# Kernel optimization log

Hardware: AMD Instinct MI355X
Metric: run time of the kernel (lower is better)

Reference implementation:

```python
import jax, jax.numpy as jnp
import numpy as np

N, K, M, DIM = 131072, 16, 128, 64


def setup_inputs() -> dict:
    key = jax.random.key(0)
    kx, ks, ka, kb = jax.random.split(key, 4)
    return {
        "x": jax.random.normal(kx, (N, DIM), dtype=jnp.float32),
        "s": jax.random.normal(ks, (K,), dtype=jnp.float32),
        "a": jax.random.normal(ka, (K, M, DIM), dtype=jnp.float32),
        "b": jax.random.normal(kb, (K, M), dtype=jnp.float32),
    }


def reference(x, s, a, b):
    # scores[k, n, m] = x[n, :] @ a[k, m, :] + b[k, m]  (batched GEMM over k)
    scores = jnp.einsum("nd,kmd->knm", x, a) + b[:, None, :]
    # per-expert logsumexp over the m affine pieces -> [k, n]
    lse = jax.nn.logsumexp(scores, axis=-1)
    # signed sum over experts -> [n]
    return jnp.einsum("k,kn->n", s, lse)
```

## Files before the change

kernel.cpp:

```cpp
#include <hip/hip_runtime.h>
#include <hip/hip_bf16.h>

#define NROWS 131072
#define KEXP 16
#define MPC 128
#define DIMD 64

typedef float f32x4  __attribute__((ext_vector_type(4)));
typedef float f32x16 __attribute__((ext_vector_type(16)));
typedef short s16x8  __attribute__((ext_vector_type(8)));

#define L2E 1.4426950408889634f
#define LN2 0.6931471805599453f

static __device__ inline unsigned int b2u(__hip_bfloat162 h) {
    union { __hip_bfloat162 h; unsigned int u; } c;
    c.h = h;
    return c.u;
}

static __device__ inline int4 cvt8s(float4 f0, float4 f1, float sc) {
    __hip_bfloat162 p0 = __float22bfloat162_rn(make_float2(f0.x * sc, f0.y * sc));
    __hip_bfloat162 p1 = __float22bfloat162_rn(make_float2(f0.z * sc, f0.w * sc));
    __hip_bfloat162 p2 = __float22bfloat162_rn(make_float2(f1.x * sc, f1.y * sc));
    __hip_bfloat162 p3 = __float22bfloat162_rn(make_float2(f1.z * sc, f1.w * sc));
    int4 pk;
    pk.x = (int)b2u(p0); pk.y = (int)b2u(p1); pk.z = (int)b2u(p2); pk.w = (int)b2u(p3);
    return pk;
}

__global__ __launch_bounds__(256, 2)
void fused_kernel(const float* __restrict__ x, const float* __restrict__ s,
                  const float* __restrict__ a, const float* __restrict__ b,
                  float* __restrict__ out) {
    __shared__ int4  abuf[2][1024];
    __shared__ float lb[KEXP * MPC];

    const int tid  = threadIdx.x;
    const int w    = tid >> 6;
    const int l    = tid & 63;
    const int ln   = l & 31;
    const int half = l >> 5;

    const int r0 = blockIdx.x * 256 + w * 64;

    {
        const float* bp = b + tid * 8;
        float4 b0 = *(const float4*)(bp);
        float4 b1 = *(const float4*)(bp + 4);
        float4 o0 = {b0.x * L2E, b0.y * L2E, b0.z * L2E, b0.w * L2E};
        float4 o1 = {b1.x * L2E, b1.y * L2E, b1.z * L2E, b1.w * L2E};
        *(float4*)(lb + tid * 8)     = o0;
        *(float4*)(lb + tid * 8 + 4) = o1;
    }

    union { int4 i; s16x8 v; } Bf[2][4];
#pragma unroll
    for (int nt = 0; nt < 2; ++nt)
#pragma unroll
        for (int c = 0; c < 4; ++c) {
            const float* gp = x + (size_t)(r0 + nt * 32 + ln) * DIMD + c * 16 + half * 8;
            float4 f0 = *(const float4*)(gp);
            float4 f1 = *(const float4*)(gp + 4);
            Bf[nt][c].i = cvt8s(f0, f1, 1.0f);
        }

#pragma unroll
    for (int i = 0; i < 4; ++i) {
        const int u  = i * 256 + tid;
        const int fb = u >> 6;
        const int ul = u & 63;
        const float* p = a + (size_t)((fb >> 2) * 32 + (ul & 31)) * DIMD
                           + (fb & 3) * 16 + (ul >> 5) * 8;
        float4 f0 = *(const float4*)(p);
        float4 f1 = *(const float4*)(p + 4);
        abuf[0][u] = cvt8s(f0, f1, L2E);
    }
    __syncthreads();

    float racc0 = 0.f, racc1 = 0.f;

    for (int k = 0; k < KEXP; ++k) {
        float4 ga[8];
        if (k + 1 < KEXP) {
            const float* ap = a + (size_t)(k + 1) * MPC * DIMD;
#pragma unroll
            for (int i = 0; i < 4; ++i) {
                const int u  = i * 256 + tid;
                const int fb = u >> 6;
                const int ul = u & 63;
                const float* p = ap + (size_t)((fb >> 2) * 32 + (ul & 31)) * DIMD
                                    + (fb & 3) * 16 + (ul >> 5) * 8;
                ga[i * 2]     = *(const float4*)(p);
                ga[i * 2 + 1] = *(const float4*)(p + 4);
            }
        }

        const int   kb  = k & 1;
        const float sk2 = s[k] * LN2;
        float esum0 = 0.f, esum1 = 0.f;

#pragma unroll
        for (int mt = 0; mt < 4; ++mt) {
            f32x4 lbv[4];
#pragma unroll
            for (int g = 0; g < 4; ++g)
                lbv[g] = *(const f32x4*)(lb + k * MPC + mt * 32 + g * 8 + half * 4);

            s16x8 Af[4];
#pragma unroll
            for (int c = 0; c < 4; ++c)
                Af[c] = *(const s16x8*)&abuf[kb][mt * 256 + c * 64 + l];

            f32x16 acc0, acc1;
#pragma unroll
            for (int g = 0; g < 4; ++g)
#pragma unroll
                for (int j = 0; j < 4; ++j) {
                    acc0[g * 4 + j] = lbv[g][j];
                    acc1[g * 4 + j] = lbv[g][j];
                }
#pragma unroll
            for (int c = 0; c < 4; ++c)
                acc0 = __builtin_amdgcn_mfma_f32_32x32x16_bf16(Af[c], Bf[0][c].v, acc0, 0, 0, 0);
#pragma unroll
            for (int c = 0; c < 4; ++c)
                acc1 = __builtin_amdgcn_mfma_f32_32x32x16_bf16(Af[c], Bf[1][c].v, acc1, 0, 0, 0);

            float e0 = 0.f, e1 = 0.f;
            {
                float t0[8], t1[8];
#pragma unroll
                for (int r = 0; r < 8; ++r) {
                    t0[r] = __builtin_amdgcn_exp2f(acc0[2 * r]) + __builtin_amdgcn_exp2f(acc0[2 * r + 1]);
                    t1[r] = __builtin_amdgcn_exp2f(acc1[2 * r]) + __builtin_amdgcn_exp2f(acc1[2 * r + 1]);
                }
#pragma unroll
                for (int r = 0; r < 4; ++r) { t0[r] += t0[r + 4]; t1[r] += t1[r + 4]; }
                e0 = (t0[0] + t0[1]) + (t0[2] + t0[3]);
                e1 = (t1[0] + t1[1]) + (t1[2] + t1[3]);
            }
            esum0 += e0;
            esum1 += e1;
        }

        float tot0 = esum0 + __shfl_xor(esum0, 32);
        float tot1 = esum1 + __shfl_xor(esum1, 32);
        racc0 = fmaf(sk2, __log2f(tot0), racc0);
        racc1 = fmaf(sk2, __log2f(tot1), racc1);

        if (k + 1 < KEXP) {
#pragma unroll
            for (int i = 0; i < 4; ++i)
                abuf[kb ^ 1][i * 256 + tid] = cvt8s(ga[i * 2], ga[i * 2 + 1], L2E);
        }
        __syncthreads();
    }

    out[r0 + l] = half ? racc1 : racc0;
}

extern "C" void kernel_launch(void* const* d_in, const int* in_sizes, int n_in,
                              void* d_out, int out_size, void* d_ws, size_t ws_size,
                              hipStream_t stream) {
    const float* x = (const float*)d_in[0];
    const float* s = (const float*)d_in[1];
    const float* a = (const float*)d_in[2];
    const float* b = (const float*)d_in[3];
    float* out = (float*)d_out;

    fused_kernel<<<NROWS / 256, 256, 0, stream>>>(x, s, a, b, out);
}
```

Measured before the change: 135.1 us.

## Pre-convert expert weights once and split experts across two block families

Adds a prep kernel that converts the expert matrices `a` to pre-swizzled bf16 (scaled by log2 e) and prescales `b` into a workspace, so the main kernel no longer converts fp32 weights per block. The main kernel streams this bf16 data into LDS with async global-to-LDS copies. It also splits the 16 experts across two block families per row tile, doubling the grid and raising the occupancy hint, and combines the two partial sums with atomicAdd after a memset of the output. This trades redundant conversion work for an extra launch, a memset, the atomics, and the x tile being read and converted twice.

```diff
diff --git a/kernel.cpp b/kernel.cpp
--- a/kernel.cpp
+++ b/kernel.cpp
@@ -29,9 +29,40 @@
     return pk;
 }
 
-__global__ __launch_bounds__(256, 2)
+static __device__ inline void async_copy16(const void* g, void* l) {
+    __builtin_amdgcn_global_load_lds(
+        (const __attribute__((address_space(1))) unsigned int*)g,
+        (__attribute__((address_space(3))) unsigned int*)l, 16, 0, 0);
+}
+
+__global__ void prep_kernel(const float* __restrict__ a, const float* __restrict__ b,
+                            short* __restrict__ abff, float* __restrict__ lbf) {
+    if (blockIdx.x < 64) {
+        const int u   = blockIdx.x * 256 + threadIdx.x;
+        const int k   = u >> 10;
+        const int rem = u & 1023;
+        const int fb  = rem >> 6;
+        const int ul  = rem & 63;
+        const int mt  = fb >> 2, c = fb & 3;
+        const float* p = a + (size_t)(k * MPC + mt * 32 + (ul & 31)) * DIMD
+                           + c * 16 + (ul >> 5) * 8;
+        float4 f0 = *(const float4*)(p);
+        float4 f1 = *(const float4*)(p + 4);
+        *(int4*)(abff + (size_t)u * 8) = cvt8s(f0, f1, L2E);
+    } else {
+        const int t = threadIdx.x;
+        float4 v0 = *(const float4*)(b + t * 8);
+        float4 v1 = *(const float4*)(b + t * 8 + 4);
+        float4 o0 = {v0.x * L2E, v0.y * L2E, v0.z * L2E, v0.w * L2E};
+        float4 o1 = {v1.x * L2E, v1.y * L2E, v1.z * L2E, v1.w * L2E};
+        *(float4*)(lbf + t * 8)     = o0;
+        *(float4*)(lbf + t * 8 + 4) = o1;
+    }
+}
+
+__global__ __launch_bounds__(256, 4)
 void fused_kernel(const float* __restrict__ x, const float* __restrict__ s,
-                  const float* __restrict__ a, const float* __restrict__ b,
+                  const short* __restrict__ abff, const float* __restrict__ lbf,
                   float* __restrict__ out) {
     __shared__ int4  abuf[2][1024];
     __shared__ float lb[KEXP * MPC];
@@ -42,16 +73,14 @@
     const int ln   = l & 31;
     const int half = l >> 5;
 
-    const int r0 = blockIdx.x * 256 + w * 64;
+    const int family = blockIdx.x & 1;
+    const int r0w    = (blockIdx.x >> 1) * 256 + w * 64;
 
     {
-        const float* bp = b + tid * 8;
-        float4 b0 = *(const float4*)(bp);
-        float4 b1 = *(const float4*)(bp + 4);
-        float4 o0 = {b0.x * L2E, b0.y * L2E, b0.z * L2E, b0.w * L2E};
-        float4 o1 = {b1.x * L2E, b1.y * L2E, b1.z * L2E, b1.w * L2E};
-        *(float4*)(lb + tid * 8)     = o0;
-        *(float4*)(lb + tid * 8 + 4) = o1;
+        float4 v0 = *(const float4*)(lbf + tid * 8);
+        float4 v1 = *(const float4*)(lbf + tid * 8 + 4);
+        *(float4*)(lb + tid * 8)     = v0;
+        *(float4*)(lb + tid * 8 + 4) = v1;
     }
 
     union { int4 i; s16x8 v; } Bf[2][4];
@@ -59,89 +88,74 @@
     for (int nt = 0; nt < 2; ++nt)
 #pragma unroll
         for (int c = 0; c < 4; ++c) {
-            const float* gp = x + (size_t)(r0 + nt * 32 + ln) * DIMD + c * 16 + half * 8;
+            const float* gp = x + (size_t)(r0w + nt * 32 + ln) * DIMD + c * 16 + half * 8;
             float4 f0 = *(const float4*)(gp);
             float4 f1 = *(const float4*)(gp + 4);
             Bf[nt][c].i = cvt8s(f0, f1, 1.0f);
         }
 
+    {
+        const short* src = abff + (size_t)(family * 8) * 8192;
 #pragma unroll
-    for (int i = 0; i < 4; ++i) {
-        const int u  = i * 256 + tid;
-        const int fb = u >> 6;
-        const int ul = u & 63;
-        const float* p = a + (size_t)((fb >> 2) * 32 + (ul & 31)) * DIMD
-                           + (fb & 3) * 16 + (ul >> 5) * 8;
-        float4 f0 = *(const float4*)(p);
-        float4 f1 = *(const float4*)(p + 4);
-        abuf[0][u] = cvt8s(f0, f1, L2E);
+        for (int i = 0; i < 4; ++i) {
+            const int chunk = w * 4 + i;
+            async_copy16(src + chunk * 512 + l * 8,
+                         (char*)&abuf[0][0] + chunk * 1024);
+        }
     }
     __syncthreads();
 
     float racc0 = 0.f, racc1 = 0.f;
 
-    for (int k = 0; k < KEXP; ++k) {
-        float4 ga[8];
-        if (k + 1 < KEXP) {
-            const float* ap = a + (size_t)(k + 1) * MPC * DIMD;
+    for (int k = 0; k < 8; ++k) {
+        const int kf = family * 8 + k;
+        const int kb = k & 1;
+
+        if (k + 1 < 8) {
+            const short* src = abff + (size_t)(kf + 1) * 8192;
 #pragma unroll
             for (int i = 0; i < 4; ++i) {
-                const int u  = i * 256 + tid;
-                const int fb = u >> 6;
-                const int ul = u & 63;
-                const float* p = ap + (size_t)((fb >> 2) * 32 + (ul & 31)) * DIMD
-                                    + (fb & 3) * 16 + (ul >> 5) * 8;
-                ga[i * 2]     = *(const float4*)(p);
-                ga[i * 2 + 1] = *(const float4*)(p + 4);
+                const int chunk = w * 4 + i;
+                async_copy16(src + chunk * 512 + l * 8,
+                             (char*)&abuf[kb ^ 1][0] + chunk * 1024);
             }
         }
 
-        const int   kb  = k & 1;
-        const float sk2 = s[k] * LN2;
+        const float sk2 = s[kf] * LN2;
         float esum0 = 0.f, esum1 = 0.f;
 
 #pragma unroll
         for (int mt = 0; mt < 4; ++mt) {
-            f32x4 lbv[4];
-#pragma unroll
-            for (int g = 0; g < 4; ++g)
-                lbv[g] = *(const f32x4*)(lb + k * MPC + mt * 32 + g * 8 + half * 4);
-
             s16x8 Af[4];
 #pragma unroll
             for (int c = 0; c < 4; ++c)
-                Af[c] = *(const s16x8*)&abuf[kb][mt * 256 + c * 64 + l];
+                Af[c] = *(const s16x8*)((const short*)&abuf[kb][0] + (mt * 4 + c) * 512 + l * 8);
 
-            f32x16 acc0, acc1;
+            union { f32x4 q[4]; f32x16 v; } acc_a, acc_b;
 #pragma unroll
-            for (int g = 0; g < 4; ++g)
-#pragma unroll
-                for (int j = 0; j < 4; ++j) {
-                    acc0[g * 4 + j] = lbv[g][j];
-                    acc1[g * 4 + j] = lbv[g][j];
-                }
+            for (int g = 0; g < 4; ++g) {
+                f32x4 t = *(const f32x4*)(lb + kf * MPC + mt * 32 + g * 8 + half * 4);
+                acc_a.q[g] = t;
+                acc_b.q[g] = t;
+            }
+
 #pragma unroll
             for (int c = 0; c < 4; ++c)
-                acc0 = __builtin_amdgcn_mfma_f32_32x32x16_bf16(Af[c], Bf[0][c].v, acc0, 0, 0, 0);
+                acc_a.v = __builtin_amdgcn_mfma_f32_32x32x16_bf16(Af[c], Bf[0][c].v, acc_a.v, 0, 0, 0);
 #pragma unroll
             for (int c = 0; c < 4; ++c)
-                acc1 = __builtin_amdgcn_mfma_f32_32x32x16_bf16(Af[c], Bf[1][c].v, acc1, 0, 0, 0);
+                acc_b.v = __builtin_amdgcn_mfma_f32_32x32x16_bf16(Af[c], Bf[1][c].v, acc_b.v, 0, 0, 0);
 
-            float e0 = 0.f, e1 = 0.f;
-            {
-                float t0[8], t1[8];
+            float ta[8], tb[8];
 #pragma unroll
-                for (int r = 0; r < 8; ++r) {
-                    t0[r] = __builtin_amdgcn_exp2f(acc0[2 * r]) + __builtin_amdgcn_exp2f(acc0[2 * r + 1]);
-                    t1[r] = __builtin_amdgcn_exp2f(acc1[2 * r]) + __builtin_amdgcn_exp2f(acc1[2 * r + 1]);
-                }
+            for (int r = 0; r < 8; ++r) {
+                ta[r] = __builtin_amdgcn_exp2f(acc_a.v[2 * r]) + __builtin_amdgcn_exp2f(acc_a.v[2 * r + 1]);
+                tb[r] = __builtin_amdgcn_exp2f(acc_b.v[2 * r]) + __builtin_amdgcn_exp2f(acc_b.v[2 * r + 1]);
+            }
 #pragma unroll
-                for (int r = 0; r < 4; ++r) { t0[r] += t0[r + 4]; t1[r] += t1[r + 4]; }
-                e0 = (t0[0] + t0[1]) + (t0[2] + t0[3]);
-                e1 = (t1[0] + t1[1]) + (t1[2] + t1[3]);
-            }
-            esum0 += e0;
-            esum1 += e1;
+            for (int r = 0; r < 4; ++r) { ta[r] += ta[r + 4]; tb[r] += tb[r + 4]; }
+            esum0 += (ta[0] + ta[1]) + (ta[2] + ta[3]);
+            esum1 += (tb[0] + tb[1]) + (tb[2] + tb[3]);
         }
 
         float tot0 = esum0 + __shfl_xor(esum0, 32);
@@ -149,15 +163,10 @@
         racc0 = fmaf(sk2, __log2f(tot0), racc0);
         racc1 = fmaf(sk2, __log2f(tot1), racc1);
 
-        if (k + 1 < KEXP) {
-#pragma unroll
-            for (int i = 0; i < 4; ++i)
-                abuf[kb ^ 1][i * 256 + tid] = cvt8s(ga[i * 2], ga[i * 2 + 1], L2E);
-        }
         __syncthreads();
     }
 
-    out[r0 + l] = half ? racc1 : racc0;
+    atomicAdd(&out[r0w + half * 32 + ln], half ? racc1 : racc0);
 }
 
 extern "C" void kernel_launch(void* const* d_in, const int* in_sizes, int n_in,
@@ -169,5 +178,10 @@
     const float* b = (const float*)d_in[3];
     float* out = (float*)d_out;
 
-    fused_kernel<<<NROWS / 256, 256, 0, stream>>>(x, s, a, b, out);
+    short* abff = (short*)d_ws;
+    float* lbf  = (float*)((char*)d_ws + 262144);
+
+    hipMemsetAsync(d_out, 0, (size_t)NROWS * sizeof(float), stream);
+    prep_kernel<<<65, 256, 0, stream>>>(a, b, abff, lbf);
+    fused_kernel<<<NROWS / 128, 256, 0, stream>>>(x, s, abff, lbf, out);
 }
```

Result: slower. 170.0 us (+25.8%).
